# Optimization experiments

Measured on AMD Instinct MI355X. Metric: run time of the kernel, lower is better.

Reference implementation:

```python
import jax, jax.numpy as jnp
import numpy as np

B, S, D = 2, 2048, 1024
H = 16
HD = D // H

def setup_inputs() -> dict:
    key = jax.random.key(0)
    ks = jax.random.split(key, 9)
    scale = 1.0 / np.sqrt(D)
    return {
        "qi": jax.random.normal(ks[0], (B, S, D), jnp.float32),
        "ki": jax.random.normal(ks[1], (B, S, D), jnp.float32),
        "vi": jax.random.normal(ks[2], (B, S, D), jnp.float32),
        "Wq": jax.random.normal(ks[3], (D, D), jnp.float32) * scale,
        "Wq_def": jax.random.normal(ks[4], (D, D), jnp.float32) * scale,
        "Wk": jax.random.normal(ks[5], (D, D), jnp.float32) * scale,
        "Wk_def": jax.random.normal(ks[6], (D, D), jnp.float32) * scale,
        "Wv": jax.random.normal(ks[7], (D, D), jnp.float32) * scale,
        "Wo": jax.random.normal(ks[8], (D, D), jnp.float32) * scale,
    }

def _heads(x, W):
    # torch Linear: x @ W.T, then view (B,S,H,HD) and transpose -> (B,H,S,HD)
    return (x @ W.T).reshape(B, S, H, HD).transpose(0, 2, 1, 3)

def reference(qi, ki, vi, Wq, Wq_def, Wk, Wk_def, Wv, Wo):
    q = _heads(qi, Wq)
    q_def = _heads(qi, Wq_def)
    k = _heads(ki, Wk)
    k_def = _heads(ki, Wk_def)
    v = _heads(vi, Wv)
    inv_sqrt = 1.0 / jnp.sqrt(jnp.asarray(HD, qi.dtype))
    scores = jnp.einsum('bhse,bhte->bhst', q, k) * inv_sqrt
    def_scores = jnp.einsum('bhse,bhte->bhst', q_def, k_def) * inv_sqrt
    # defeasible weights: sigmoid(def_scores).sum over t -> [B,H,S], broadcast over query dim
    def_w = jax.nn.sigmoid(def_scores).sum(axis=3)  # [B,H,S]
    attn = jax.nn.softmax(scores * def_w[:, :, None, :], axis=-1)
    attended = jnp.einsum('bhst,bhtd->bshd', attn, v).reshape(B, S, D)
    return attended @ Wo.T
```

## Files before the change

kernel.cpp:

```cpp
#include <hip/hip_runtime.h>
#include <math.h>

#define BSZ 2
#define SEQ 2048
#define DIM 1024
#define NH 16
#define HDIM 64
#define MR (BSZ*SEQ)

typedef __attribute__((ext_vector_type(8))) short bf16x8;
typedef __attribute__((ext_vector_type(4))) short bf16x4;
typedef __attribute__((ext_vector_type(4))) float floatx4;
typedef _Float16 f16x8 __attribute__((ext_vector_type(8)));

static __device__ __forceinline__ unsigned short f2bf(float x) {
    unsigned u = __float_as_uint(x);
    u += 0x7fffu + ((u >> 16) & 1u);
    return (unsigned short)(u >> 16);
}
static __device__ __forceinline__ float bf2f(unsigned short h) {
    return __uint_as_float(((unsigned)h) << 16);
}
static __device__ __forceinline__ unsigned short f2h(float x) {
    union { _Float16 h; unsigned short u; } v;
    v.h = (_Float16)x;
    return v.u;
}
#define MFMA16(a,b,c) __builtin_amdgcn_mfma_f32_16x16x32_bf16((a),(b),(c),0,0,0)

static __device__ __forceinline__ floatx4 mfma_f16(bf16x8 a, bf16x8 b, floatx4 c) {
    union { bf16x8 s; f16x8 h; } ua, ub;
    ua.s = a; ub.s = b;
    return __builtin_amdgcn_mfma_f32_16x16x32_f16(ua.h, ub.h, c, 0, 0, 0);
}

static __device__ __forceinline__ floatx4 pv_mfma(bf16x4 a, bf16x4 b, floatx4 c) {
#if __has_builtin(__builtin_amdgcn_mfma_f32_16x16x16bf16_1k)
    return __builtin_amdgcn_mfma_f32_16x16x16bf16_1k(a, b, c, 0, 0, 0);
#else
    bf16x8 a8 = {a[0],a[1],a[2],a[3],0,0,0,0};
    bf16x8 b8 = {b[0],b[1],b[2],b[3],0,0,0,0};
    return MFMA16(a8, b8, c);
#endif
}

__global__ __launch_bounds__(256)
void conv_split(const float* p0, const float* p1, const float* p2,
                const float* p3,
                unsigned short* o0, unsigned short* o1, unsigned short* o2,
                unsigned short* o3,
                int r0, int r1, int r2, int r3)
{
    const float* pin; unsigned short* pout; int rows;
    switch (blockIdx.y) {
        case 0: pin=p0; pout=o0; rows=r0; break;
        case 1: pin=p1; pout=o1; rows=r1; break;
        case 2: pin=p2; pout=o2; rows=r2; break;
        default: pin=p3; pout=o3; rows=r3; break;
    }
    size_t idx = (size_t)blockIdx.x * 256 + threadIdx.x;
    if (idx * 4 >= (size_t)rows * DIM) return;
    size_t row = (idx * 4) >> 10;
    int col = (int)((idx * 4) & 1023);
    float4 f = *(const float4*)(pin + idx * 4);
    ushort4 h, l;
    h.x = f2bf(f.x); l.x = f2bf(f.x - bf2f(h.x));
    h.y = f2bf(f.y); l.y = f2bf(f.y - bf2f(h.y));
    h.z = f2bf(f.z); l.z = f2bf(f.z - bf2f(h.z));
    h.w = f2bf(f.w); l.w = f2bf(f.w - bf2f(h.w));
    *(ushort4*)(pout + row * 2048 + col)        = h;
    *(ushort4*)(pout + row * 2048 + 1024 + col) = l;
}

__global__ __launch_bounds__(256)
void conv_f16(const float* p0, const float* p1, const float* p2, const float* p3,
              unsigned short* o0, unsigned short* o1, unsigned short* o2,
              unsigned short* o3, int r0, int r1, int r2, int r3)
{
    const float* pin; unsigned short* pout; int rows;
    switch (blockIdx.y) {
        case 0: pin=p0; pout=o0; rows=r0; break;
        case 1: pin=p1; pout=o1; rows=r1; break;
        case 2: pin=p2; pout=o2; rows=r2; break;
        default: pin=p3; pout=o3; rows=r3; break;
    }
    size_t idx = (size_t)blockIdx.x * 256 + threadIdx.x;
    if (idx * 4 >= (size_t)rows * DIM) return;
    float4 f = *(const float4*)(pin + idx * 4);
    ushort4 h;
    h.x = f2h(f.x); h.y = f2h(f.y); h.z = f2h(f.z); h.w = f2h(f.w);
    *(ushort4*)(pout + idx * 4) = h;
}

__global__ __launch_bounds__(256)
void conv_hi(const float* p0, const float* p1, const float* p2,
             unsigned short* o0, unsigned short* o1, unsigned short* o2,
             int n0, int n1, int n2)
{
    const float* pin; unsigned short* pout; int n;
    switch (blockIdx.y) {
        case 0: pin=p0; pout=o0; n=n0; break;
        case 1: pin=p1; pout=o1; n=n1; break;
        default: pin=p2; pout=o2; n=n2; break;
    }
    size_t idx = (size_t)blockIdx.x * 256 + threadIdx.x;
    if (idx * 4 >= (size_t)n) return;
    float4 f = *(const float4*)(pin + idx * 4);
    ushort4 h;
    h.x = f2bf(f.x); h.y = f2bf(f.y); h.z = f2bf(f.z); h.w = f2bf(f.w);
    *(ushort4*)(pout + idx * 4) = h;
}

template<int EPI, bool SPLIT3, int DT>
__global__ __launch_bounds__(256)
void gemm_mfma(const unsigned short* __restrict__ A0, const unsigned short* __restrict__ A1,
               const unsigned short* __restrict__ B0, const unsigned short* __restrict__ B1,
               void* C0v, void* C1v, int lda, int ldb, int nkb)
{
    const unsigned short* A = blockIdx.z ? A1 : A0;
    const unsigned short* B = blockIdx.z ? B1 : B0;
    float* Cf = (float*)(blockIdx.z ? C1v : C0v);
    unsigned short* Cb = (unsigned short*)(blockIdx.z ? C1v : C0v);

    __shared__ __align__(16) unsigned short As[128][72];
    __shared__ __align__(16) unsigned short Bs[128][72];

    const int tid = threadIdx.x;
    const int lane = tid & 63, wv = tid >> 6;
    const int c = lane & 15, quad = lane >> 4;
    const int wm = wv >> 1, wn = wv & 1;
    const int rowBase = blockIdx.y << 7;
    const int colBase = blockIdx.x << 7;

    floatx4 acc[4][4];
#pragma unroll
    for (int i = 0; i < 4; ++i)
#pragma unroll
        for (int j = 0; j < 4; ++j) acc[i][j] = (floatx4){0.f,0.f,0.f,0.f};

    bf16x8 ar[4], br[4];
    {
#pragma unroll
        for (int i = 0; i < 4; ++i) {
            int f = tid + (i << 8);
            int r = f >> 3, kbk = (f & 7) << 3;
            ar[i] = *(const bf16x8*)(A + (size_t)(rowBase + r) * lda + kbk);
            br[i] = *(const bf16x8*)(B + (size_t)(colBase + r) * ldb + kbk);
        }
    }
    for (int kb = 0; kb < nkb; ++kb) {
        __syncthreads();
#pragma unroll
        for (int i = 0; i < 4; ++i) {
            int f = tid + (i << 8);
            int r = f >> 3, kbk = (f & 7) << 3;
            *(bf16x8*)&As[r][kbk] = ar[i];
            *(bf16x8*)&Bs[r][kbk] = br[i];
        }
        __syncthreads();
        if (kb + 1 < nkb) {
            int kn = kb + 1, aoff, boff;
            if (SPLIT3) {
                int t = kn >> 4, kk = (kn & 15) << 6;
                aoff = ((t == 1) ? 1024 : 0) + kk;
                boff = ((t == 2) ? 1024 : 0) + kk;
            } else { aoff = boff = kn << 6; }
#pragma unroll
            for (int i = 0; i < 4; ++i) {
                int f = tid + (i << 8);
                int r = f >> 3, kbk = (f & 7) << 3;
                ar[i] = *(const bf16x8*)(A + (size_t)(rowBase + r) * lda + aoff + kbk);
                br[i] = *(const bf16x8*)(B + (size_t)(colBase + r) * ldb + boff + kbk);
            }
        }
#pragma unroll
        for (int ks = 0; ks < 2; ++ks) {
            bf16x8 af[4], bfr[4];
#pragma unroll
            for (int i = 0; i < 4; ++i) {
                af[i]  = *(const bf16x8*)&As[wm*64 + i*16 + c][ks*32 + quad*8];
                bfr[i] = *(const bf16x8*)&Bs[wn*64 + i*16 + c][ks*32 + quad*8];
            }
#pragma unroll
            for (int mi = 0; mi < 4; ++mi)
#pragma unroll
                for (int ni = 0; ni < 4; ++ni) {
                    if (DT == 0) acc[mi][ni] = MFMA16(af[mi], bfr[ni], acc[mi][ni]);
                    else         acc[mi][ni] = mfma_f16(af[mi], bfr[ni], acc[mi][ni]);
                }
        }
    }
    const int row0 = rowBase + wm*64 + quad*4;
    if (EPI == 0) {
        const int col0 = colBase + wn*64 + c;
#pragma unroll
        for (int mi = 0; mi < 4; ++mi)
#pragma unroll
            for (int r = 0; r < 4; ++r) {
                size_t ro = (size_t)(row0 + mi*16 + r) * 1024 + col0;
#pragma unroll
                for (int ni = 0; ni < 4; ++ni)
                    Cf[ro + ni*16] = acc[mi][ni][r];
            }
    } else if (EPI == 1) {
        const int h = (colBase >> 6) + wn;
#pragma unroll
        for (int mi = 0; mi < 4; ++mi)
#pragma unroll
            for (int r = 0; r < 4; ++r) {
                int row = row0 + mi*16 + r;
                int b = row >> 11, s = row & 2047;
                size_t base = ((size_t)((b<<4) | h) * 2048 + s) * 128;
#pragma unroll
                for (int ni = 0; ni < 4; ++ni) {
                    int d = ni*16 + c;
                    float x = acc[mi][ni][r];
                    unsigned short hb = f2bf(x);
                    Cb[base + d]      = hb;
                    Cb[base + 64 + d] = f2bf(x - bf2f(hb));
                }
            }
    } else if (EPI == 2) {
        const int h = (colBase >> 6) + wn;
#pragma unroll
        for (int mi = 0; mi < 4; ++mi) {
            int row = row0 + mi*16;
            int b = row >> 11, s = row & 2047;
#pragma unroll
            for (int ni = 0; ni < 4; ++ni) {
                int d = ni*16 + c;
                size_t base = ((size_t)((b<<4)|h) * 64 + d) * 2048 + s;
                ushort4 o4;
                o4.x = f2bf(acc[mi][ni][0]); o4.y = f2bf(acc[mi][ni][1]);
                o4.z = f2bf(acc[mi][ni][2]); o4.w = f2bf(acc[mi][ni][3]);
                *(ushort4*)(Cb + base) = o4;
            }
        }
    } else {
        const int h = (colBase >> 6) + wn;
#pragma unroll
        for (int mi = 0; mi < 4; ++mi)
#pragma unroll
            for (int r = 0; r < 4; ++r) {
                int row = row0 + mi*16 + r;
                int b = row >> 11, s = row & 2047;
                size_t base = ((size_t)((b<<4) | h) * 2048 + s) * 64;
#pragma unroll
                for (int ni = 0; ni < 4; ++ni)
                    Cb[base + ni*16 + c] = f2h(acc[mi][ni][r]);
            }
    }
}

__global__ __launch_bounds__(256)
void defw_mfma(const unsigned short* __restrict__ qd,
               const unsigned short* __restrict__ kd,
               float* __restrict__ defw)
{
    __shared__ __align__(16) unsigned short Ks[64][72];
    const int tid = threadIdx.x;
    const int wv = tid >> 6, lane = tid & 63;
    const int c = lane & 15, quad = lane >> 4;
    const int bh = blockIdx.y;
    const int qbase = blockIdx.x << 7;
    const int trow = tid >> 2, seg = tid & 3;

    bf16x8 qf[2][2];
#pragma unroll
    for (int mi = 0; mi < 2; ++mi) {
        const unsigned short* qrow =
            qd + ((size_t)bh*2048 + qbase + wv*32 + mi*16 + c)*64 + quad*8;
        qf[mi][0] = *(const bf16x8*)(qrow);
        qf[mi][1] = *(const bf16x8*)(qrow + 32);
    }
    float rs[2][4] = {{0.f,0.f,0.f,0.f},{0.f,0.f,0.f,0.f}};
    const unsigned short* kbase = kd + (size_t)bh*2048*64;
    bf16x8 kpre[2];
    {
        const unsigned short* kp = kbase + (size_t)trow*64 + seg*16;
        kpre[0] = *(const bf16x8*)(kp);
        kpre[1] = *(const bf16x8*)(kp + 8);
    }
    for (int kt = 0; kt < SEQ; kt += 64) {
        __syncthreads();
        *(bf16x8*)&Ks[trow][seg*16 + 0] = kpre[0];
        *(bf16x8*)&Ks[trow][seg*16 + 8] = kpre[1];
        __syncthreads();
        if (kt + 64 < SEQ) {
            const unsigned short* kp = kbase + (size_t)(kt + 64 + trow)*64 + seg*16;
            kpre[0] = *(const bf16x8*)(kp);
            kpre[1] = *(const bf16x8*)(kp + 8);
        }
#pragma unroll
        for (int nk = 0; nk < 4; ++nk) {
            const unsigned short* kr = &Ks[16*nk + c][quad*8];
            bf16x8 k0 = *(const bf16x8*)(kr);
            bf16x8 k1 = *(const bf16x8*)(kr + 32);
#pragma unroll
            for (int mi = 0; mi < 2; ++mi) {
                floatx4 s = {0.f,0.f,0.f,0.f};
                s = mfma_f16(qf[mi][0], k0, s);
                s = mfma_f16(qf[mi][1], k1, s);
#pragma unroll
                for (int r = 0; r < 4; ++r)
                    rs[mi][r] += 1.f / (1.f + __expf(-0.125f * s[r]));
            }
        }
    }
#pragma unroll
    for (int mi = 0; mi < 2; ++mi)
#pragma unroll
        for (int r = 0; r < 4; ++r) {
            float vv = rs[mi][r];
            vv += __shfl_xor(vv, 1, 16);
            vv += __shfl_xor(vv, 2, 16);
            vv += __shfl_xor(vv, 4, 16);
            vv += __shfl_xor(vv, 8, 16);
            if (c == 0)
                defw[(size_t)bh*SEQ + qbase + wv*32 + mi*16 + 4*quad + r]
                    = vv * 0.125f;
        }
}

__global__ __launch_bounds__(256)
void flash_mfma(const unsigned short* __restrict__ q,
                const unsigned short* __restrict__ kk,
                const unsigned short* __restrict__ vt,
                const float* __restrict__ dwg,
                unsigned short* __restrict__ o)
{
    __shared__ __align__(16) unsigned short Ks[64][136];
    __shared__ __align__(16) unsigned short Vs[64][72];
    const int tid = threadIdx.x;
    const int wv = tid >> 6, lane = tid & 63;
    const int c = lane & 15, quad = lane >> 4;
    const int bh = blockIdx.y, b = bh >> 4, h = bh & 15;
    const int qbase = blockIdx.x << 7;
    const int trow = tid >> 2, seg = tid & 3;

    bf16x8 qhi[2][2], qlo[2][2];
#pragma unroll
    for (int mi = 0; mi < 2; ++mi) {
        const unsigned short* qrow =
            q + ((size_t)bh*2048 + qbase + wv*32 + mi*16 + c)*128 + quad*8;
        qhi[mi][0] = *(const bf16x8*)(qrow);
        qhi[mi][1] = *(const bf16x8*)(qrow + 32);
        qlo[mi][0] = *(const bf16x8*)(qrow + 64);
        qlo[mi][1] = *(const bf16x8*)(qrow + 96);
    }
    floatx4 Oa[4][2];
#pragma unroll
    for (int nd = 0; nd < 4; ++nd)
#pragma unroll
        for (int mi = 0; mi < 2; ++mi) Oa[nd][mi] = (floatx4){0.f,0.f,0.f,0.f};
    float mrun[2] = {-3.0e38f, -3.0e38f}, lrun[2] = {0.f, 0.f};

    const unsigned short* kbase = kk + (size_t)bh*2048*128;
    const unsigned short* vbase = vt + (size_t)bh*64*2048;

    bf16x8 kpre[4], vpre[2];
    {
        const unsigned short* kp = kbase + (size_t)trow*128 + seg*32;
#pragma unroll
        for (int u = 0; u < 4; ++u) kpre[u] = *(const bf16x8*)(kp + 8*u);
        const unsigned short* vp = vbase + (size_t)trow*2048 + seg*16;
        vpre[0] = *(const bf16x8*)(vp);
        vpre[1] = *(const bf16x8*)(vp + 8);
    }

    for (int kt = 0; kt < SEQ; kt += 64) {
        __syncthreads();
#pragma unroll
        for (int u = 0; u < 4; ++u) *(bf16x8*)&Ks[trow][seg*32 + 8*u] = kpre[u];
        *(bf16x8*)&Vs[trow][seg*16 + 0] = vpre[0];
        *(bf16x8*)&Vs[trow][seg*16 + 8] = vpre[1];
        float dwf[4][4];
#pragma unroll
        for (int nk = 0; nk < 4; ++nk) {
            float4 d4 = *(const float4*)&dwg[(size_t)bh*SEQ + kt + nk*16 + quad*4];
            dwf[nk][0]=d4.x; dwf[nk][1]=d4.y; dwf[nk][2]=d4.z; dwf[nk][3]=d4.w;
        }
        __syncthreads();
        if (kt + 64 < SEQ) {
            const unsigned short* kp = kbase + (size_t)(kt + 64 + trow)*128 + seg*32;
#pragma unroll
            for (int u = 0; u < 4; ++u) kpre[u] = *(const bf16x8*)(kp + 8*u);
            const unsigned short* vp = vbase + (size_t)trow*2048 + (kt + 64) + seg*16;
            vpre[0] = *(const bf16x8*)(vp);
            vpre[1] = *(const bf16x8*)(vp + 8);
        }

        float z[2][4][4];
#pragma unroll
        for (int nk = 0; nk < 4; ++nk) {
            const unsigned short* kr = &Ks[16*nk + c][quad*8];
            bf16x8 kh0 = *(const bf16x8*)(kr);
            bf16x8 kh1 = *(const bf16x8*)(kr + 32);
            bf16x8 kl0 = *(const bf16x8*)(kr + 64);
            bf16x8 kl1 = *(const bf16x8*)(kr + 96);
#pragma unroll
            for (int mi = 0; mi < 2; ++mi) {
                floatx4 s = {0.f,0.f,0.f,0.f};
                s = MFMA16(kh0, qhi[mi][0], s);
                s = MFMA16(kh1, qhi[mi][1], s);
                s = MFMA16(kh0, qlo[mi][0], s);
                s = MFMA16(kh1, qlo[mi][1], s);
                s = MFMA16(kl0, qhi[mi][0], s);
                s = MFMA16(kl1, qhi[mi][1], s);
#pragma unroll
                for (int r = 0; r < 4; ++r) z[mi][nk][r] = s[r] * dwf[nk][r];
            }
        }
        float alpha[2];
#pragma unroll
        for (int mi = 0; mi < 2; ++mi) {
            float tm = z[mi][0][0];
#pragma unroll
            for (int nk = 0; nk < 4; ++nk)
#pragma unroll
                for (int r = 0; r < 4; ++r) tm = fmaxf(tm, z[mi][nk][r]);
            tm = fmaxf(tm, __shfl_xor(tm, 16));
            tm = fmaxf(tm, __shfl_xor(tm, 32));
            float mn = fmaxf(mrun[mi], tm);
            alpha[mi] = __expf(mrun[mi] - mn);
            mrun[mi] = mn;
            float rsum = 0.f;
#pragma unroll
            for (int nk = 0; nk < 4; ++nk)
#pragma unroll
                for (int r = 0; r < 4; ++r) {
                    z[mi][nk][r] = __expf(z[mi][nk][r] - mn);
                    rsum += z[mi][nk][r];
                }
            rsum += __shfl_xor(rsum, 16);
            rsum += __shfl_xor(rsum, 32);
            lrun[mi] = lrun[mi] * alpha[mi] + rsum;
        }
        bf16x4 pb[2][4];
#pragma unroll
        for (int mi = 0; mi < 2; ++mi)
#pragma unroll
            for (int nk = 0; nk < 4; ++nk) {
                bf16x4 p;
                p[0] = (short)f2bf(z[mi][nk][0]);
                p[1] = (short)f2bf(z[mi][nk][1]);
                p[2] = (short)f2bf(z[mi][nk][2]);
                p[3] = (short)f2bf(z[mi][nk][3]);
                pb[mi][nk] = p;
            }
#pragma unroll
        for (int nd = 0; nd < 4; ++nd)
#pragma unroll
            for (int mi = 0; mi < 2; ++mi)
#pragma unroll
                for (int r = 0; r < 4; ++r)
                    Oa[nd][mi][r] *= alpha[mi];
#pragma unroll
        for (int ks = 0; ks < 4; ++ks)
#pragma unroll
            for (int nd = 0; nd < 4; ++nd) {
                bf16x4 va = *(const bf16x4*)&Vs[nd*16 + c][ks*16 + quad*4];
#pragma unroll
                for (int mi = 0; mi < 2; ++mi)
                    Oa[nd][mi] = pv_mfma(va, pb[mi][ks], Oa[nd][mi]);
            }
    }
#pragma unroll
    for (int mi = 0; mi < 2; ++mi) {
        float invl = 1.f / lrun[mi];
        int s_abs = qbase + wv*32 + mi*16 + c;
        unsigned short* orow = o + ((size_t)(b*SEQ + s_abs))*DIM + h*HDIM;
#pragma unroll
        for (int nd = 0; nd < 4; ++nd) {
            ushort4 o4;
            o4.x = f2bf(Oa[nd][mi][0] * invl);
            o4.y = f2bf(Oa[nd][mi][1] * invl);
            o4.z = f2bf(Oa[nd][mi][2] * invl);
            o4.w = f2bf(Oa[nd][mi][3] * invl);
            *(ushort4*)(orow + nd*16 + quad*4) = o4;
        }
    }
}

extern "C" void kernel_launch(void* const* d_in, const int* in_sizes, int n_in,
                              void* d_out, int out_size, void* d_ws, size_t ws_size,
                              hipStream_t stream)
{
    (void)in_sizes; (void)n_in; (void)out_size; (void)ws_size;
    const float* qi     = (const float*)d_in[0];
    const float* ki     = (const float*)d_in[1];
    const float* vi     = (const float*)d_in[2];
    const float* Wq     = (const float*)d_in[3];
    const float* Wq_def = (const float*)d_in[4];
    const float* Wk     = (const float*)d_in[5];
    const float* Wk_def = (const float*)d_in[6];
    const float* Wv     = (const float*)d_in[7];
    const float* Wo     = (const float*)d_in[8];
    float* out = (float*)d_out;

    char* ws = (char*)d_ws;
    const size_t MB = 1024 * 1024;
    unsigned short* Aqf  = (unsigned short*)(ws +  0*MB);
    unsigned short* Akf  = (unsigned short*)(ws +  8*MB);
    unsigned short* Bqdf = (unsigned short*)(ws + 16*MB);
    unsigned short* Bkdf = (unsigned short*)(ws + 18*MB);
    unsigned short* qdf  = (unsigned short*)(ws + 20*MB);
    unsigned short* kdf  = (unsigned short*)(ws + 28*MB);
    unsigned short* Aq  = (unsigned short*)(ws +  0*MB);
    unsigned short* Ak  = (unsigned short*)(ws + 16*MB);
    unsigned short* Bq  = (unsigned short*)(ws + 32*MB);
    unsigned short* Bk  = (unsigned short*)(ws + 36*MB);
    unsigned short* qs  = (unsigned short*)(ws + 40*MB);
    unsigned short* ks  = (unsigned short*)(ws + 56*MB);
    float*          dw  = (float*)(ws + 72*MB);
    unsigned short* Av  = (unsigned short*)(ws +  0*MB);
    unsigned short* Bv  = (unsigned short*)(ws +  8*MB);
    unsigned short* Bo  = (unsigned short*)(ws + 10*MB);
    unsigned short* Vt  = (unsigned short*)(ws + 12*MB);
    unsigned short* att = (unsigned short*)(ws + 20*MB);

    dim3 cb(256);
    dim3 gP(DIM/128, MR/128, 2);
    dim3 gS(DIM/128, MR/128, 1);
    dim3 gA(SEQ/128, BSZ*NH);

    conv_f16<<<dim3(4096, 4), cb, 0, stream>>>(
        qi, ki, Wq_def, Wk_def, Aqf, Akf, Bqdf, Bkdf, MR, MR, DIM, DIM);
    gemm_mfma<3, false, 1><<<gP, cb, 0, stream>>>(Aqf, Akf, Bqdf, Bkdf, qdf, kdf, 1024, 1024, 16);
    defw_mfma<<<gA, cb, 0, stream>>>(qdf, kdf, dw);
    conv_split<<<dim3(4096, 4), cb, 0, stream>>>(
        qi, ki, Wq, Wk, Aq, Ak, Bq, Bk, MR, MR, DIM, DIM);
    gemm_mfma<1, true, 0><<<gP, cb, 0, stream>>>(Aq, Ak, Bq, Bk, qs, ks, 2048, 2048, 48);
    conv_hi<<<dim3(4096, 3), cb, 0, stream>>>(vi, Wv, Wo, Av, Bv, Bo,
                                              MR*DIM, DIM*DIM, DIM*DIM);
    gemm_mfma<2, false, 0><<<gS, cb, 0, stream>>>(Av, Av, Bv, Bv, Vt, Vt, 1024, 1024, 16);
    flash_mfma<<<gA, cb, 0, stream>>>(qs, ks, Vt, dw, att);
    gemm_mfma<0, false, 0><<<gS, cb, 0, stream>>>(att, att, Bo, Bo, out, out, 1024, 1024, 16);
}
```

Measured before the change: 438.5 us.

## Double-buffer K/V tiles via direct global-to-LDS loads with XOR swizzle

The flash attention kernel now streams K and V tiles straight into double-buffered LDS using global_load_lds, with manual vmcnt waits and raw barriers replacing the register-staged prefetch. The projection epilogues write K and V^T in an XOR-swizzled layout so the unpadded LDS tiles avoid bank conflicts. The defeasible weights for the whole head are preloaded into LDS. The softmax switches to exp2 by folding log2(e) into the weight scale and skips the O/l rescale when no row max grows. This adds LDS footprint and tight coupling between the producer layout and the consumer indexing, and the vmcnt counts must match the number of loads in flight.

Result: slower. 451.5 us (+3.0%).

```diff
diff --git a/kernel.cpp b/kernel.cpp
--- a/kernel.cpp
+++ b/kernel.cpp
@@ -42,6 +42,12 @@
     bf16x8 b8 = {b[0],b[1],b[2],b[3],0,0,0,0};
     return MFMA16(a8, b8, c);
 #endif
+}
+
+static __device__ __forceinline__ void gld16(const void* g, void* l) {
+    __builtin_amdgcn_global_load_lds(
+        (const __attribute__((address_space(1))) void*)g,
+        (__attribute__((address_space(3))) void*)l, 16, 0, 0);
 }
 
 __global__ __launch_bounds__(256)
@@ -211,13 +217,15 @@
                 int row = row0 + mi*16 + r;
                 int b = row >> 11, s = row & 2047;
                 size_t base = ((size_t)((b<<4) | h) * 2048 + s) * 128;
+                const int sw = (s & 7) << 3;
 #pragma unroll
                 for (int ni = 0; ni < 4; ++ni) {
                     int d = ni*16 + c;
+                    int dsw = d ^ sw;
                     float x = acc[mi][ni][r];
                     unsigned short hb = f2bf(x);
-                    Cb[base + d]      = hb;
-                    Cb[base + 64 + d] = f2bf(x - bf2f(hb));
+                    Cb[base + dsw]      = hb;
+                    Cb[base + 64 + dsw] = f2bf(x - bf2f(hb));
                 }
             }
     } else if (EPI == 2) {
@@ -229,7 +237,8 @@
 #pragma unroll
             for (int ni = 0; ni < 4; ++ni) {
                 int d = ni*16 + c;
-                size_t base = ((size_t)((b<<4)|h) * 64 + d) * 2048 + s;
+                int scol = s ^ ((d & 7) << 3);
+                size_t base = ((size_t)((b<<4)|h) * 64 + d) * 2048 + scol;
                 ushort4 o4;
                 o4.x = f2bf(acc[mi][ni][0]); o4.y = f2bf(acc[mi][ni][1]);
                 o4.z = f2bf(acc[mi][ni][2]); o4.w = f2bf(acc[mi][ni][3]);
@@ -318,7 +327,7 @@
             vv += __shfl_xor(vv, 8, 16);
             if (c == 0)
                 defw[(size_t)bh*SEQ + qbase + wv*32 + mi*16 + 4*quad + r]
-                    = vv * 0.125f;
+                    = vv * 0.18033688011112042f;
         }
 }
 
@@ -329,25 +338,50 @@
                 const float* __restrict__ dwg,
                 unsigned short* __restrict__ o)
 {
-    __shared__ __align__(16) unsigned short Ks[64][136];
-    __shared__ __align__(16) unsigned short Vs[64][72];
+    __shared__ __align__(16) unsigned short Ks[2][64][128];
+    __shared__ __align__(16) unsigned short Vs[2][64][64];
+    __shared__ __align__(16) float dwL[SEQ];
     const int tid = threadIdx.x;
     const int wv = tid >> 6, lane = tid & 63;
     const int c = lane & 15, quad = lane >> 4;
+    const int cswz = c & 7;
     const int bh = blockIdx.y, b = bh >> 4, h = bh & 15;
     const int qbase = blockIdx.x << 7;
-    const int trow = tid >> 2, seg = tid & 3;
+
+    const unsigned short* kbase = kk + (size_t)bh*2048*128;
+    const unsigned short* vbase = vt + (size_t)bh*64*2048;
 
     bf16x8 qhi[2][2], qlo[2][2];
 #pragma unroll
     for (int mi = 0; mi < 2; ++mi) {
         const unsigned short* qrow =
-            q + ((size_t)bh*2048 + qbase + wv*32 + mi*16 + c)*128 + quad*8;
-        qhi[mi][0] = *(const bf16x8*)(qrow);
-        qhi[mi][1] = *(const bf16x8*)(qrow + 32);
-        qlo[mi][0] = *(const bf16x8*)(qrow + 64);
-        qlo[mi][1] = *(const bf16x8*)(qrow + 96);
-    }
+            q + ((size_t)bh*2048 + qbase + wv*32 + mi*16 + c)*128;
+        qhi[mi][0] = *(const bf16x8*)(qrow + (((quad     ) ^ cswz) << 3));
+        qhi[mi][1] = *(const bf16x8*)(qrow + (((quad +  4) ^ cswz) << 3));
+        qlo[mi][0] = *(const bf16x8*)(qrow + (((quad +  8) ^ cswz) << 3));
+        qlo[mi][1] = *(const bf16x8*)(qrow + (((quad + 12) ^ cswz) << 3));
+    }
+#pragma unroll
+    for (int i = 0; i < 2; ++i) {
+        int flat = tid + (i << 8);
+        gld16(dwg + (size_t)bh*SEQ + (size_t)flat*4,
+              &dwL[(wv*64 + (i << 8)) * 4]);
+    }
+#pragma unroll
+    for (int i = 0; i < 4; ++i) {
+        int flat = tid + (i << 8);
+        int r = flat >> 4, ch = flat & 15;
+        gld16(kbase + (size_t)r*128 + (ch << 3),
+              &Ks[0][0][0] + ((wv*64 + (i << 8)) << 3));
+    }
+#pragma unroll
+    for (int i = 0; i < 2; ++i) {
+        int flat = tid + (i << 8);
+        int d = flat >> 3, ch = flat & 7;
+        gld16(vbase + (size_t)d*2048 + (ch << 3),
+              &Vs[0][0][0] + ((wv*64 + (i << 8)) << 3));
+    }
+
     floatx4 Oa[4][2];
 #pragma unroll
     for (int nd = 0; nd < 4; ++nd)
@@ -355,49 +389,41 @@
         for (int mi = 0; mi < 2; ++mi) Oa[nd][mi] = (floatx4){0.f,0.f,0.f,0.f};
     float mrun[2] = {-3.0e38f, -3.0e38f}, lrun[2] = {0.f, 0.f};
 
-    const unsigned short* kbase = kk + (size_t)bh*2048*128;
-    const unsigned short* vbase = vt + (size_t)bh*64*2048;
-
-    bf16x8 kpre[4], vpre[2];
-    {
-        const unsigned short* kp = kbase + (size_t)trow*128 + seg*32;
-#pragma unroll
-        for (int u = 0; u < 4; ++u) kpre[u] = *(const bf16x8*)(kp + 8*u);
-        const unsigned short* vp = vbase + (size_t)trow*2048 + seg*16;
-        vpre[0] = *(const bf16x8*)(vp);
-        vpre[1] = *(const bf16x8*)(vp + 8);
-    }
-
     for (int kt = 0; kt < SEQ; kt += 64) {
-        __syncthreads();
-#pragma unroll
-        for (int u = 0; u < 4; ++u) *(bf16x8*)&Ks[trow][seg*32 + 8*u] = kpre[u];
-        *(bf16x8*)&Vs[trow][seg*16 + 0] = vpre[0];
-        *(bf16x8*)&Vs[trow][seg*16 + 8] = vpre[1];
-        float dwf[4][4];
+        const int cur = (kt >> 6) & 1;
+        __builtin_amdgcn_s_barrier();
+        if (kt + 64 < SEQ) {
+            const int nb = cur ^ 1;
+#pragma unroll
+            for (int i = 0; i < 4; ++i) {
+                int flat = tid + (i << 8);
+                int r = flat >> 4, ch = flat & 15;
+                gld16(kbase + (size_t)(kt + 64 + r)*128 + (ch << 3),
+                      &Ks[nb][0][0] + ((wv*64 + (i << 8)) << 3));
+            }
+#pragma unroll
+            for (int i = 0; i < 2; ++i) {
+                int flat = tid + (i << 8);
+                int d = flat >> 3, ch = flat & 7;
+                gld16(vbase + (size_t)d*2048 + (kt + 64) + (ch << 3),
+                      &Vs[nb][0][0] + ((wv*64 + (i << 8)) << 3));
+            }
+            asm volatile("s_waitcnt vmcnt(6)" ::: "memory");
+        } else {
+            asm volatile("s_waitcnt vmcnt(0)" ::: "memory");
+        }
+        __builtin_amdgcn_s_barrier();
+        __builtin_amdgcn_sched_barrier(0);
+
+        float z[2][4][4];
 #pragma unroll
         for (int nk = 0; nk < 4; ++nk) {
-            float4 d4 = *(const float4*)&dwg[(size_t)bh*SEQ + kt + nk*16 + quad*4];
-            dwf[nk][0]=d4.x; dwf[nk][1]=d4.y; dwf[nk][2]=d4.z; dwf[nk][3]=d4.w;
-        }
-        __syncthreads();
-        if (kt + 64 < SEQ) {
-            const unsigned short* kp = kbase + (size_t)(kt + 64 + trow)*128 + seg*32;
-#pragma unroll
-            for (int u = 0; u < 4; ++u) kpre[u] = *(const bf16x8*)(kp + 8*u);
-            const unsigned short* vp = vbase + (size_t)trow*2048 + (kt + 64) + seg*16;
-            vpre[0] = *(const bf16x8*)(vp);
-            vpre[1] = *(const bf16x8*)(vp + 8);
-        }
-
-        float z[2][4][4];
-#pragma unroll
-        for (int nk = 0; nk < 4; ++nk) {
-            const unsigned short* kr = &Ks[16*nk + c][quad*8];
-            bf16x8 kh0 = *(const bf16x8*)(kr);
-            bf16x8 kh1 = *(const bf16x8*)(kr + 32);
-            bf16x8 kl0 = *(const bf16x8*)(kr + 64);
-            bf16x8 kl1 = *(const bf16x8*)(kr + 96);
+            const unsigned short* krow = &Ks[cur][16*nk + c][0];
+            bf16x8 kh0 = *(const bf16x8*)(krow + (((quad     ) ^ cswz) << 3));
+            bf16x8 kh1 = *(const bf16x8*)(krow + (((quad +  4) ^ cswz) << 3));
+            bf16x8 kl0 = *(const bf16x8*)(krow + (((quad +  8) ^ cswz) << 3));
+            bf16x8 kl1 = *(const bf16x8*)(krow + (((quad + 12) ^ cswz) << 3));
+            float4 d4 = *(const float4*)&dwL[kt + nk*16 + quad*4];
 #pragma unroll
             for (int mi = 0; mi < 2; ++mi) {
                 floatx4 s = {0.f,0.f,0.f,0.f};
@@ -407,11 +433,12 @@
                 s = MFMA16(kh1, qlo[mi][1], s);
                 s = MFMA16(kl0, qhi[mi][0], s);
                 s = MFMA16(kl1, qhi[mi][1], s);
-#pragma unroll
-                for (int r = 0; r < 4; ++r) z[mi][nk][r] = s[r] * dwf[nk][r];
-            }
-        }
-        float alpha[2];
+                z[mi][nk][0] = s[0] * d4.x;
+                z[mi][nk][1] = s[1] * d4.y;
+                z[mi][nk][2] = s[2] * d4.z;
+                z[mi][nk][3] = s[3] * d4.w;
+            }
+        }
 #pragma unroll
         for (int mi = 0; mi < 2; ++mi) {
             float tm = z[mi][0][0];
@@ -421,20 +448,28 @@
                 for (int r = 0; r < 4; ++r) tm = fmaxf(tm, z[mi][nk][r]);
             tm = fmaxf(tm, __shfl_xor(tm, 16));
             tm = fmaxf(tm, __shfl_xor(tm, 32));
-            float mn = fmaxf(mrun[mi], tm);
-            alpha[mi] = __expf(mrun[mi] - mn);
-            mrun[mi] = mn;
+            if (__any(tm > mrun[mi])) {
+                float mn = fmaxf(mrun[mi], tm);
+                float al = exp2f(mrun[mi] - mn);
+                mrun[mi] = mn;
+                lrun[mi] *= al;
+#pragma unroll
+                for (int nd = 0; nd < 4; ++nd)
+#pragma unroll
+                    for (int r = 0; r < 4; ++r)
+                        Oa[nd][mi][r] *= al;
+            }
             float rsum = 0.f;
 #pragma unroll
             for (int nk = 0; nk < 4; ++nk)
 #pragma unroll
                 for (int r = 0; r < 4; ++r) {
-                    z[mi][nk][r] = __expf(z[mi][nk][r] - mn);
+                    z[mi][nk][r] = exp2f(z[mi][nk][r] - mrun[mi]);
                     rsum += z[mi][nk][r];
                 }
             rsum += __shfl_xor(rsum, 16);
             rsum += __shfl_xor(rsum, 32);
-            lrun[mi] = lrun[mi] * alpha[mi] + rsum;
+            lrun[mi] += rsum;
         }
         bf16x4 pb[2][4];
 #pragma unroll
@@ -449,21 +484,17 @@
                 pb[mi][nk] = p;
             }
 #pragma unroll
-        for (int nd = 0; nd < 4; ++nd)
-#pragma unroll
-            for (int mi = 0; mi < 2; ++mi)
-#pragma unroll
-                for (int r = 0; r < 4; ++r)
-                    Oa[nd][mi][r] *= alpha[mi];
-#pragma unroll
-        for (int ks = 0; ks < 4; ++ks)
+        for (int ks = 0; ks < 4; ++ks) {
+            const int vch = ((2*ks + (quad >> 1)) ^ cswz);
 #pragma unroll
             for (int nd = 0; nd < 4; ++nd) {
-                bf16x4 va = *(const bf16x4*)&Vs[nd*16 + c][ks*16 + quad*4];
+                const bf16x4 va = *(const bf16x4*)
+                    (&Vs[cur][nd*16 + c][0] + (vch << 3) + ((quad & 1) << 2));
 #pragma unroll
                 for (int mi = 0; mi < 2; ++mi)
                     Oa[nd][mi] = pv_mfma(va, pb[mi][ks], Oa[nd][mi]);
             }
+        }
     }
 #pragma unroll
     for (int mi = 0; mi < 2; ++mi) {
```
